# Performance work log

Hardware: AMD Instinct MI355X
Metric: run time of the kernel (lower is better)

## Reference

```python
import jax, jax.numpy as jnp
import numpy as np

EPS = 1e-5
PROJ_EPS = 1e-5
MAX_TANH_ARG = 15.0
NUM_LAYERS = 2

def _norm(x):
    return jnp.sqrt(jnp.sum(x * x, axis=-1, keepdims=True))

def log_map_zero(y):
    # Poincare ball log map at the origin: arctanh(||y||) * y / ||y||
    n = _norm(y)
    n_c = jnp.clip(n, EPS, 1.0 - PROJ_EPS)
    return jnp.arctanh(n_c) * y / jnp.maximum(n, EPS)

def exp_map_zero(v):
    # Poincare ball exp map at the origin: tanh(||v||) * v / ||v||
    n = _norm(v)
    n_c = jnp.clip(n, EPS, MAX_TANH_ARG)
    return jnp.tanh(n_c) * v / jnp.maximum(n, EPS)

def setup_inputs() -> dict:
    key = jax.random.key(0)
    k1, k2, k3, k4 = jax.random.split(key, 4)
    N, K, D = 50000, 32, 128
    # scale initial features so they lie inside the unit ball
    node_repr = jax.random.normal(k1, (N, D), dtype=jnp.float32) * 0.01
    adj_mat = jax.random.randint(k2, (N, K), 0, N, dtype=jnp.int32)
    weight = jax.random.uniform(k3, (N, K), dtype=jnp.float32)
    mask = jnp.ones((N, 1), dtype=jnp.float32)
    # learned params: one [D, D] matrix per layer (tie_weight=False, poincare)
    msg_weights = jax.random.normal(k4, (NUM_LAYERS, D, D), dtype=jnp.float32) * (1.0 / np.sqrt(D))
    return {"node_repr": node_repr, "adj_mat": adj_mat, "weight": weight,
            "mask": mask, "msg_weights": msg_weights}

def reference(node_repr, adj_mat, weight, mask, msg_weights):
    x = node_repr
    for step in range(NUM_LAYERS):
        # log map back to tangent space at origin (identity on first layer)
        x = (log_map_zero(x) if step > 0 else x) * mask
        msg = (x @ msg_weights[step]) * mask            # [N, D] dense projection
        nbr = msg[adj_mat]                              # [N, K, D] gather by adjacency
        combined = jnp.einsum('nk,nkd->nd', weight, nbr) * mask  # weighted neighbor sum (dropout p=0)
        x = exp_map_zero(combined) * mask               # back to the manifold
        x = jax.nn.relu(x) * mask                       # poincare activation
    return x
```

## Files before the change

### kernel.cpp

```cpp
#include <hip/hip_runtime.h>

#define EPS 1e-5f
#define PROJ_EPS 1e-5f
#define MAX_TANH_ARG 15.0f

typedef __bf16 bf16x8 __attribute__((ext_vector_type(8)));
typedef float f32x4 __attribute__((ext_vector_type(4)));
typedef float f32x2 __attribute__((ext_vector_type(2)));

__device__ __forceinline__ unsigned short f2bf(float f) {
  unsigned u = __builtin_bit_cast(unsigned, f);
  u += 0x7fffu + ((u >> 16) & 1u);
  return (unsigned short)(u >> 16);
}

union BF8 {
  unsigned short u[8];
  bf16x8 v;
  uint4 q;
};

__global__ __launch_bounds__(256) void prep_kernel(
    const float* __restrict__ W, unsigned short* __restrict__ wpack) {
  const int tid = blockIdx.x * 256 + threadIdx.x;
  if (tid >= 4096) return;
  const int l = tid & 63;
  const int s = (tid >> 6) & 3;
  const int tt = (tid >> 8) & 7;
  const int layer = tid >> 11;
  const int q2 = l >> 4;
  const int n = tt * 16 + (l & 15);
  unsigned short* dst = wpack + ((size_t)((layer * 32 + tt * 4 + s) * 64 + l)) * 8;
  const float* src = W + (size_t)layer * 16384;
#pragma unroll
  for (int j = 0; j < 8; ++j) {
    const int k = s * 32 + q2 * 8 + j;
    dst[j] = f2bf(src[(size_t)k * 128 + n]);
  }
}

__global__ __launch_bounds__(256) void gemm0_kernel(
    const float* __restrict__ xf, const float* __restrict__ mask,
    const unsigned short* __restrict__ wpack, unsigned short* __restrict__ msg,
    const int* __restrict__ adj, const float* __restrict__ wgt,
    unsigned* __restrict__ edges, int nedge, int N, int planeBytes) {
  __shared__ unsigned short tile[64][136];
  const int t = threadIdx.x;
  const int lane = t & 63;
  const int wv = t >> 6;
  const int m = lane & 15;
  const int quad = lane >> 4;
  const int base = blockIdx.x * 64;
  const int wbase = base + wv * 16;

#pragma unroll
  for (int i = 0; i < 8; ++i) {
    const int ge = base * 32 + i * 256 + t;
    if (ge < nedge) {
      const unsigned id = (unsigned)adj[ge] & 0xffffu;
      const unsigned short h = __builtin_bit_cast(unsigned short, (_Float16)wgt[ge]);
      edges[ge] = id | ((unsigned)h << 16);
    }
  }

  {
    const int r = lane >> 2;
    const int c = (lane & 3) * 32;
    const int gr = wbase + r;
    const int grc = gr < N ? gr : N - 1;
    const float4* src = (const float4*)(xf + (size_t)grc * 128 + c);
    unsigned short* drow = &tile[wv * 16 + r][c];
#pragma unroll
    for (int i = 0; i < 8; ++i) {
      const float4 p = src[i];
      drow[i * 4 + 0] = f2bf(p.x);
      drow[i * 4 + 1] = f2bf(p.y);
      drow[i * 4 + 2] = f2bf(p.z);
      drow[i * 4 + 3] = f2bf(p.w);
    }
  }

  f32x4 acc[8];
#pragma unroll
  for (int tt = 0; tt < 8; ++tt) acc[tt] = (f32x4){0.f, 0.f, 0.f, 0.f};
#pragma unroll
  for (int sk = 0; sk < 4; ++sk) {
    BF8 a;
    a.q = *(const uint4*)&tile[wv * 16 + m][sk * 32 + quad * 8];
#pragma unroll
    for (int tt = 0; tt < 8; ++tt) {
      BF8 b;
      b.q = *(const uint4*)(wpack + (size_t)((tt * 4 + sk) * 64 + lane) * 8);
      acc[tt] = __builtin_amdgcn_mfma_f32_16x16x32_bf16(a.v, b.v, acc[tt], 0, 0, 0);
    }
  }

  float sc[4];
#pragma unroll
  for (int r = 0; r < 4; ++r) {
    int rr = wbase + quad * 4 + r;
    rr = rr < N ? rr : N - 1;
    const float s = mask[rr];
    sc[r] = s * s;
  }
#pragma unroll
  for (int tt = 0; tt < 8; ++tt) {
    const int c = tt * 16 + m;
#pragma unroll
    for (int r = 0; r < 4; ++r)
      tile[wv * 16 + quad * 4 + r][c] = f2bf(acc[tt][r] * sc[r]);
  }
  const int r16 = lane >> 2;
  const int sub2 = lane & 3;
  const int grow = wbase + r16;
  if (grow < N) {
#pragma unroll
    for (int p = 0; p < 4; ++p) {
      *(uint4*)((char*)msg + (size_t)p * planeBytes + (size_t)grow * 64 + sub2 * 16) =
          *(const uint4*)((const char*)&tile[wv * 16 + r16][0] + p * 64 + sub2 * 16);
    }
  }
}

__global__ __launch_bounds__(256, 3) void agg_gemm1_kernel(
    const unsigned short* __restrict__ msg, const unsigned* __restrict__ edges,
    const float* __restrict__ mask, const unsigned short* __restrict__ wpack2,
    unsigned short* __restrict__ msg2, int N, int planeBytes) {
  __shared__ unsigned short tile[64][136];
  __shared__ float sAll[64];
  __shared__ float sRel[64];
  const int t = threadIdx.x;
  const int lane = t & 63;
  const int wv = t >> 6;
  const int nbase = blockIdx.x * 64;
  const int wrow0 = wv * 16;
  const int pstart = blockIdx.x & 3;

  const int node = lane >> 2;
  const int sub = lane & 3;
  const int suboff = sub * 16;
  const int gn0 = nbase + wrow0 + node;
  const int gnc = gn0 < N ? gn0 : N - 1;

  unsigned ew[32];
#pragma unroll
  for (int i = 0; i < 8; ++i)
    *(uint4*)&ew[4 * i] = *(const uint4*)(edges + (size_t)gnc * 32 + i * 4);

  float s_all = 0.f, s_rel = 0.f;

#pragma unroll
  for (int phse = 0; phse < 4; ++phse) {
    const int p = (pstart + phse) & 3;
    const char* plane = (const char*)msg + (size_t)p * planeBytes;

    f32x2 acc[4];
#pragma unroll
    for (int d = 0; d < 4; ++d) acc[d] = (f32x2){0.f, 0.f};

    uint4 q[16];
#pragma unroll
    for (int k = 0; k < 16; ++k)
      q[k] = *(const uint4*)(plane + ((size_t)(ew[k] & 0xffffu) * 64 + suboff));

#pragma unroll
    for (int k = 0; k < 16; ++k) {
      const float w = (float)__builtin_bit_cast(_Float16, (unsigned short)(ew[k] >> 16));
      const f32x2 w2 = {w, w};
      const uint4 qq = q[k];
      q[k] = *(const uint4*)(plane + ((size_t)(ew[16 + k] & 0xffffu) * 64 + suboff));
#pragma unroll
      for (int d = 0; d < 4; ++d) {
        const unsigned qd = (&qq.x)[d];
        f32x2 v2;
        v2.x = __builtin_bit_cast(float, qd << 16);
        v2.y = __builtin_bit_cast(float, qd & 0xffff0000u);
        acc[d] = __builtin_elementwise_fma(v2, w2, acc[d]);
      }
    }
#pragma unroll
    for (int k = 0; k < 16; ++k) {
      const float w = (float)__builtin_bit_cast(_Float16,
                                                (unsigned short)(ew[16 + k] >> 16));
      const f32x2 w2 = {w, w};
#pragma unroll
      for (int d = 0; d < 4; ++d) {
        const unsigned qd = (&q[k].x)[d];
        f32x2 v2;
        v2.x = __builtin_bit_cast(float, qd << 16);
        v2.y = __builtin_bit_cast(float, qd & 0xffff0000u);
        acc[d] = __builtin_elementwise_fma(v2, w2, acc[d]);
      }
    }

    uint4 pk4;
    unsigned* pw = &pk4.x;
#pragma unroll
    for (int d = 0; d < 4; ++d) {
      s_all = fmaf(acc[d].x, acc[d].x, s_all);
      s_all = fmaf(acc[d].y, acc[d].y, s_all);
      const float r0 = fmaxf(acc[d].x, 0.f);
      const float r1 = fmaxf(acc[d].y, 0.f);
      s_rel = fmaf(r0, r0, s_rel);
      s_rel = fmaf(r1, r1, s_rel);
      pw[d] = (unsigned)f2bf(r0) | ((unsigned)f2bf(r1) << 16);
    }
    *(uint4*)&tile[wrow0 + node][p * 32 + sub * 8] = pk4;
  }

  s_all += __shfl_xor(s_all, 1);
  s_all += __shfl_xor(s_all, 2);
  s_rel += __shfl_xor(s_rel, 1);
  s_rel += __shfl_xor(s_rel, 2);
  if (sub == 0) {
    sAll[wrow0 + node] = s_all;
    sRel[wrow0 + node] = s_rel;
  }

  const int m = lane & 15;
  const int quad = lane >> 4;
  f32x4 gacc[8];
#pragma unroll
  for (int tt = 0; tt < 8; ++tt) gacc[tt] = (f32x4){0.f, 0.f, 0.f, 0.f};
#pragma unroll
  for (int sk = 0; sk < 4; ++sk) {
    BF8 a;
    a.q = *(const uint4*)&tile[wrow0 + m][sk * 32 + quad * 8];
#pragma unroll
    for (int tt = 0; tt < 8; ++tt) {
      BF8 b;
      b.q = *(const uint4*)(wpack2 + (size_t)((tt * 4 + sk) * 64 + lane) * 8);
      gacc[tt] = __builtin_amdgcn_mfma_f32_16x16x32_bf16(a.v, b.v, gacc[tt], 0, 0, 0);
    }
  }

  float sc[4];
#pragma unroll
  for (int r = 0; r < 4; ++r) {
    const int lr = wrow0 + quad * 4 + r;
    int rr = nbase + lr;
    rr = rr < N ? rr : N - 1;
    const float mm = mask[rr];
    const float S_all = sAll[lr];
    const float S_rel = sRel[lr];
    const float s2 = mm * mm * S_all;
    const float nrm = sqrtf(s2);
    const float ncl = fminf(fmaxf(nrm, EPS), MAX_TANH_ARG);
    const float f1 = tanhf(ncl) / fmaxf(nrm, EPS) * mm * mm * mm;
    const float r2 = f1 * f1 * S_rel;
    const float nr = sqrtf(r2);
    const float nc2 = fminf(fmaxf(nr, EPS), 1.0f - PROJ_EPS);
    const float ls = 0.5f * logf((1.f + nc2) / (1.f - nc2)) / fmaxf(nr, EPS);
    sc[r] = ls * mm * mm * f1;
  }
#pragma unroll
  for (int tt = 0; tt < 8; ++tt) {
    const int c = tt * 16 + m;
#pragma unroll
    for (int r = 0; r < 4; ++r)
      tile[wrow0 + quad * 4 + r][c] = f2bf(gacc[tt][r] * sc[r]);
  }
  const int r16 = lane >> 2;
  const int sub2 = lane & 3;
  const int grow = nbase + wrow0 + r16;
  if (grow < N) {
#pragma unroll
    for (int p = 0; p < 4; ++p) {
      *(uint4*)((char*)msg2 + (size_t)p * planeBytes + (size_t)grow * 64 + sub2 * 16) =
          *(const uint4*)((const char*)&tile[wrow0 + r16][0] + p * 64 + sub2 * 16);
    }
  }
}

__global__ __launch_bounds__(256, 3) void agg_final_kernel(
    const unsigned short* __restrict__ msg2, const unsigned* __restrict__ edges,
    const float* __restrict__ mask, float* __restrict__ out, int N,
    int planeBytes) {
  const int t = threadIdx.x;
  const int lane = t & 63;
  const int wv = t >> 6;
  const int nbase = blockIdx.x * 64;
  const int wrow0 = wv * 16;
  const int pstart = blockIdx.x & 3;

  const int node = lane >> 2;
  const int sub = lane & 3;
  const int suboff = sub * 16;
  const int gnode = nbase + wrow0 + node;
  const int gnc = gnode < N ? gnode : N - 1;

  unsigned ew[32];
#pragma unroll
  for (int i = 0; i < 8; ++i)
    *(uint4*)&ew[4 * i] = *(const uint4*)(edges + (size_t)gnc * 32 + i * 4);

  f32x2 res[16];

#pragma unroll
  for (int phse = 0; phse < 4; ++phse) {
    const int p = (pstart + phse) & 3;
    const char* plane = (const char*)msg2 + (size_t)p * planeBytes;

    f32x2 acc[4];
#pragma unroll
    for (int d = 0; d < 4; ++d) acc[d] = (f32x2){0.f, 0.f};

    uint4 q[16];
#pragma unroll
    for (int k = 0; k < 16; ++k)
      q[k] = *(const uint4*)(plane + ((size_t)(ew[k] & 0xffffu) * 64 + suboff));

#pragma unroll
    for (int k = 0; k < 16; ++k) {
      const float w = (float)__builtin_bit_cast(_Float16, (unsigned short)(ew[k] >> 16));
      const f32x2 w2 = {w, w};
      const uint4 qq = q[k];
      q[k] = *(const uint4*)(plane + ((size_t)(ew[16 + k] & 0xffffu) * 64 + suboff));
#pragma unroll
      for (int d = 0; d < 4; ++d) {
        const unsigned qd = (&qq.x)[d];
        f32x2 v2;
        v2.x = __builtin_bit_cast(float, qd << 16);
        v2.y = __builtin_bit_cast(float, qd & 0xffff0000u);
        acc[d] = __builtin_elementwise_fma(v2, w2, acc[d]);
      }
    }
#pragma unroll
    for (int k = 0; k < 16; ++k) {
      const float w = (float)__builtin_bit_cast(_Float16,
                                                (unsigned short)(ew[16 + k] >> 16));
      const f32x2 w2 = {w, w};
#pragma unroll
      for (int d = 0; d < 4; ++d) {
        const unsigned qd = (&q[k].x)[d];
        f32x2 v2;
        v2.x = __builtin_bit_cast(float, qd << 16);
        v2.y = __builtin_bit_cast(float, qd & 0xffff0000u);
        acc[d] = __builtin_elementwise_fma(v2, w2, acc[d]);
      }
    }
#pragma unroll
    for (int d = 0; d < 4; ++d) res[phse * 4 + d] = acc[d];
  }

  float s_all = 0.f;
#pragma unroll
  for (int i = 0; i < 16; ++i) {
    s_all = fmaf(res[i].x, res[i].x, s_all);
    s_all = fmaf(res[i].y, res[i].y, s_all);
  }
  s_all += __shfl_xor(s_all, 1);
  s_all += __shfl_xor(s_all, 2);

  const float mm = mask[gnc];
  const float s2 = mm * mm * s_all;
  const float nrm = sqrtf(s2);
  const float ncl = fminf(fmaxf(nrm, EPS), MAX_TANH_ARG);
  const float f2 = tanhf(ncl) / fmaxf(nrm, EPS) * mm * mm * mm;

  if (gnode < N) {
    float* orow = out + (size_t)gnode * 128;
#pragma unroll
    for (int phse = 0; phse < 4; ++phse) {
      const int p = (pstart + phse) & 3;
      float4 o0, o1;
      o0.x = f2 * fmaxf(res[phse * 4 + 0].x, 0.f);
      o0.y = f2 * fmaxf(res[phse * 4 + 0].y, 0.f);
      o0.z = f2 * fmaxf(res[phse * 4 + 1].x, 0.f);
      o0.w = f2 * fmaxf(res[phse * 4 + 1].y, 0.f);
      o1.x = f2 * fmaxf(res[phse * 4 + 2].x, 0.f);
      o1.y = f2 * fmaxf(res[phse * 4 + 2].y, 0.f);
      o1.z = f2 * fmaxf(res[phse * 4 + 3].x, 0.f);
      o1.w = f2 * fmaxf(res[phse * 4 + 3].y, 0.f);
      *(float4*)(orow + p * 32 + sub * 8) = o0;
      *(float4*)(orow + p * 32 + sub * 8 + 4) = o1;
    }
  }
}

extern "C" void kernel_launch(void* const* d_in, const int* in_sizes, int n_in,
                              void* d_out, int out_size, void* d_ws, size_t ws_size,
                              hipStream_t stream) {
  const float* node = (const float*)d_in[0];
  const int* adj = (const int*)d_in[1];
  const float* wgt = (const float*)d_in[2];
  const float* mask = (const float*)d_in[3];
  const float* mw = (const float*)d_in[4];
  float* out = (float*)d_out;
  const int N = in_sizes[0] / 128;
  const int gb = (N + 63) / 64;
  const int planeBytes = gb * 64 * 64;
  const int nedge = N * 32;

  unsigned short* msg1 = (unsigned short*)d_out;
  unsigned short* wpack = (unsigned short*)d_ws;
  unsigned short* msg2 = (unsigned short*)((char*)d_ws + 65536);
  unsigned* edges = (unsigned*)((char*)d_ws + 65536 + (size_t)4 * planeBytes);

  hipLaunchKernelGGL(prep_kernel, dim3(16), dim3(256), 0, stream, mw, wpack);
  hipLaunchKernelGGL(gemm0_kernel, dim3(gb), dim3(256), 0, stream,
                     node, mask, wpack, msg1, adj, wgt, edges, nedge, N, planeBytes);
  hipLaunchKernelGGL(agg_gemm1_kernel, dim3(gb), dim3(256), 0, stream,
                     msg1, edges, mask, wpack + 16384, msg2, N, planeBytes);
  hipLaunchKernelGGL(agg_final_kernel, dim3(gb), dim3(256), 0, stream,
                     msg2, edges, mask, out, N, planeBytes);
}
```

Before: 225.0 us.

## Stage edge lists through LDS, use nontemporal streams, pin gather scheduling

Several memory-path tweaks. Each wave now loads its 16 nodes' edge lists with coalesced loads into a padded LDS buffer and reads them back per lane, instead of each lane doing strided 128-byte global loads. Streaming writes (edges, msg planes, final output) and the input feature reads use nontemporal hints so they do not pollute the cache that holds the gathered msg planes. Scheduling barriers keep the compiler from reordering the gather loads and the FMA blocks. The cost is extra LDS per block, which may reduce occupancy in the aggregation kernels, plus no barrier-free hazard: LDS is written and read within the same wave, so no syncthreads is needed.

```diff
diff --git a/kernel.cpp b/kernel.cpp
--- a/kernel.cpp
+++ b/kernel.cpp
@@ -7,6 +7,7 @@
 typedef __bf16 bf16x8 __attribute__((ext_vector_type(8)));
 typedef float f32x4 __attribute__((ext_vector_type(4)));
 typedef float f32x2 __attribute__((ext_vector_type(2)));
+typedef unsigned u32x4 __attribute__((ext_vector_type(4)));
 
 __device__ __forceinline__ unsigned short f2bf(float f) {
   unsigned u = __builtin_bit_cast(unsigned, f);
@@ -59,7 +60,7 @@
     if (ge < nedge) {
       const unsigned id = (unsigned)adj[ge] & 0xffffu;
       const unsigned short h = __builtin_bit_cast(unsigned short, (_Float16)wgt[ge]);
-      edges[ge] = id | ((unsigned)h << 16);
+      __builtin_nontemporal_store(id | ((unsigned)h << 16), &edges[ge]);
     }
   }
 
@@ -68,11 +69,11 @@
     const int c = (lane & 3) * 32;
     const int gr = wbase + r;
     const int grc = gr < N ? gr : N - 1;
-    const float4* src = (const float4*)(xf + (size_t)grc * 128 + c);
+    const f32x4* src = (const f32x4*)(xf + (size_t)grc * 128 + c);
     unsigned short* drow = &tile[wv * 16 + r][c];
 #pragma unroll
     for (int i = 0; i < 8; ++i) {
-      const float4 p = src[i];
+      const f32x4 p = __builtin_nontemporal_load(src + i);
       drow[i * 4 + 0] = f2bf(p.x);
       drow[i * 4 + 1] = f2bf(p.y);
       drow[i * 4 + 2] = f2bf(p.z);
@@ -116,8 +117,9 @@
   if (grow < N) {
 #pragma unroll
     for (int p = 0; p < 4; ++p) {
-      *(uint4*)((char*)msg + (size_t)p * planeBytes + (size_t)grow * 64 + sub2 * 16) =
-          *(const uint4*)((const char*)&tile[wv * 16 + r16][0] + p * 64 + sub2 * 16);
+      const u32x4 v = *(const u32x4*)((const char*)&tile[wv * 16 + r16][0] + p * 64 + sub2 * 16);
+      __builtin_nontemporal_store(
+          v, (u32x4*)((char*)msg + (size_t)p * planeBytes + (size_t)grow * 64 + sub2 * 16));
     }
   }
 }
@@ -126,6 +128,7 @@
     const unsigned short* __restrict__ msg, const unsigned* __restrict__ edges,
     const float* __restrict__ mask, const unsigned short* __restrict__ wpack2,
     unsigned short* __restrict__ msg2, int N, int planeBytes) {
+  __shared__ unsigned ep[64 * 36];
   __shared__ unsigned short tile[64][136];
   __shared__ float sAll[64];
   __shared__ float sRel[64];
@@ -136,16 +139,24 @@
   const int wrow0 = wv * 16;
   const int pstart = blockIdx.x & 3;
 
+#pragma unroll
+  for (int i = 0; i < 8; ++i) {
+    const int idx = i * 64 + lane;
+    const int r = idx >> 5, w = idx & 31;
+    const int gn = nbase + wrow0 + r;
+    unsigned v = 0u;
+    if (gn < N) v = edges[(size_t)gn * 32 + w];
+    ep[(wrow0 + r) * 36 + w] = v;
+  }
+
   const int node = lane >> 2;
   const int sub = lane & 3;
   const int suboff = sub * 16;
-  const int gn0 = nbase + wrow0 + node;
-  const int gnc = gn0 < N ? gn0 : N - 1;
 
   unsigned ew[32];
 #pragma unroll
   for (int i = 0; i < 8; ++i)
-    *(uint4*)&ew[4 * i] = *(const uint4*)(edges + (size_t)gnc * 32 + i * 4);
+    *(uint4*)&ew[4 * i] = *(const uint4*)(ep + (wrow0 + node) * 36 + 4 * i);
 
   float s_all = 0.f, s_rel = 0.f;
 
@@ -162,6 +173,7 @@
 #pragma unroll
     for (int k = 0; k < 16; ++k)
       q[k] = *(const uint4*)(plane + ((size_t)(ew[k] & 0xffffu) * 64 + suboff));
+    __builtin_amdgcn_sched_barrier(0);
 
 #pragma unroll
     for (int k = 0; k < 16; ++k) {
@@ -178,6 +190,7 @@
         acc[d] = __builtin_elementwise_fma(v2, w2, acc[d]);
       }
     }
+    __builtin_amdgcn_sched_barrier(0);
 #pragma unroll
     for (int k = 0; k < 16; ++k) {
       const float w = (float)__builtin_bit_cast(_Float16,
@@ -266,8 +279,9 @@
   if (grow < N) {
 #pragma unroll
     for (int p = 0; p < 4; ++p) {
-      *(uint4*)((char*)msg2 + (size_t)p * planeBytes + (size_t)grow * 64 + sub2 * 16) =
-          *(const uint4*)((const char*)&tile[wrow0 + r16][0] + p * 64 + sub2 * 16);
+      const u32x4 v = *(const u32x4*)((const char*)&tile[wrow0 + r16][0] + p * 64 + sub2 * 16);
+      __builtin_nontemporal_store(
+          v, (u32x4*)((char*)msg2 + (size_t)p * planeBytes + (size_t)grow * 64 + sub2 * 16));
     }
   }
 }
@@ -276,6 +290,7 @@
     const unsigned short* __restrict__ msg2, const unsigned* __restrict__ edges,
     const float* __restrict__ mask, float* __restrict__ out, int N,
     int planeBytes) {
+  __shared__ unsigned ep[64 * 36];
   const int t = threadIdx.x;
   const int lane = t & 63;
   const int wv = t >> 6;
@@ -283,6 +298,16 @@
   const int wrow0 = wv * 16;
   const int pstart = blockIdx.x & 3;
 
+#pragma unroll
+  for (int i = 0; i < 8; ++i) {
+    const int idx = i * 64 + lane;
+    const int r = idx >> 5, w = idx & 31;
+    const int gn = nbase + wrow0 + r;
+    unsigned v = 0u;
+    if (gn < N) v = edges[(size_t)gn * 32 + w];
+    ep[(wrow0 + r) * 36 + w] = v;
+  }
+
   const int node = lane >> 2;
   const int sub = lane & 3;
   const int suboff = sub * 16;
@@ -292,7 +317,7 @@
   unsigned ew[32];
 #pragma unroll
   for (int i = 0; i < 8; ++i)
-    *(uint4*)&ew[4 * i] = *(const uint4*)(edges + (size_t)gnc * 32 + i * 4);
+    *(uint4*)&ew[4 * i] = *(const uint4*)(ep + (wrow0 + node) * 36 + 4 * i);
 
   f32x2 res[16];
 
@@ -309,6 +334,7 @@
 #pragma unroll
     for (int k = 0; k < 16; ++k)
       q[k] = *(const uint4*)(plane + ((size_t)(ew[k] & 0xffffu) * 64 + suboff));
+    __builtin_amdgcn_sched_barrier(0);
 
 #pragma unroll
     for (int k = 0; k < 16; ++k) {
@@ -325,6 +351,7 @@
         acc[d] = __builtin_elementwise_fma(v2, w2, acc[d]);
       }
     }
+    __builtin_amdgcn_sched_barrier(0);
 #pragma unroll
     for (int k = 0; k < 16; ++k) {
       const float w = (float)__builtin_bit_cast(_Float16,
@@ -363,7 +390,7 @@
 #pragma unroll
     for (int phse = 0; phse < 4; ++phse) {
       const int p = (pstart + phse) & 3;
-      float4 o0, o1;
+      f32x4 o0, o1;
       o0.x = f2 * fmaxf(res[phse * 4 + 0].x, 0.f);
       o0.y = f2 * fmaxf(res[phse * 4 + 0].y, 0.f);
       o0.z = f2 * fmaxf(res[phse * 4 + 1].x, 0.f);
@@ -372,8 +399,8 @@
       o1.y = f2 * fmaxf(res[phse * 4 + 2].y, 0.f);
       o1.z = f2 * fmaxf(res[phse * 4 + 3].x, 0.f);
       o1.w = f2 * fmaxf(res[phse * 4 + 3].y, 0.f);
-      *(float4*)(orow + p * 32 + sub * 8) = o0;
-      *(float4*)(orow + p * 32 + sub * 8 + 4) = o1;
+      __builtin_nontemporal_store(o0, (f32x4*)(orow + p * 32 + sub * 8));
+      __builtin_nontemporal_store(o1, (f32x4*)(orow + p * 32 + sub * 8 + 4));
     }
   }
 }
```

Result: slower. 246.9 us (+9.8%).
